# Kernel optimization log

Measured on AMD Instinct MI355X. Metric: run time of the kernel, lower is better.

## Reference

```python
import jax, jax.numpy as jnp
import numpy as np

EMBED_DIM = 4096
POLY_PTS = 32
POLY_DIM = POLY_PTS * 2  # 64
LN_EPS = 1e-5


def setup_inputs() -> dict:
    key = jax.random.key(0)
    ks = jax.random.split(key, 12)
    B, N, Dmax = 8, 1024, POLY_DIM
    s = 0.02
    return {
        "prompts": jax.random.normal(ks[0], (B, N, Dmax), dtype=jnp.float32),
        "prompt_types": jax.random.randint(ks[1], (B, N), 0, 3, dtype=jnp.int64),
        # point encoder: Linear(2, E)
        "point_w": jax.random.normal(ks[2], (EMBED_DIM, 2), dtype=jnp.float32) * s,
        "point_b": jax.random.normal(ks[3], (EMBED_DIM,), dtype=jnp.float32) * s,
        # box encoder: Linear(4, E)
        "box_w": jax.random.normal(ks[4], (EMBED_DIM, 4), dtype=jnp.float32) * s,
        "box_b": jax.random.normal(ks[5], (EMBED_DIM,), dtype=jnp.float32) * s,
        # polygon encoder: Linear(64,E) -> LayerNorm(E) -> ReLU -> Linear(E,E)
        "poly_w1": jax.random.normal(ks[6], (EMBED_DIM, POLY_DIM), dtype=jnp.float32) * s,
        "poly_b1": jax.random.normal(ks[7], (EMBED_DIM,), dtype=jnp.float32) * s,
        "ln_gamma": jnp.ones((EMBED_DIM,), dtype=jnp.float32),
        "ln_beta": jnp.zeros((EMBED_DIM,), dtype=jnp.float32),
        "poly_w2": jax.random.normal(ks[8], (EMBED_DIM, EMBED_DIM), dtype=jnp.float32) * s,
        "poly_b2": jax.random.normal(ks[9], (EMBED_DIM,), dtype=jnp.float32) * s,
        # type embedding table (3, E)
        "type_emb": jax.random.normal(ks[10], (3, EMBED_DIM), dtype=jnp.float32) * s,
    }


def _layernorm(x, gamma, beta):
    mu = jnp.mean(x, axis=-1, keepdims=True)
    var = jnp.mean(jnp.square(x - mu), axis=-1, keepdims=True)
    return (x - mu) * jax.lax.rsqrt(var + LN_EPS) * gamma + beta


def reference(prompts, prompt_types, point_w, point_b, box_w, box_b,
              poly_w1, poly_b1, ln_gamma, ln_beta, poly_w2, poly_b2, type_emb):
    # Per-type expert encodings computed densely, then selected by type mask
    # (same math as torch's masked gather -> linear -> scatter).
    pt = jnp.einsum('bnd,ed->bne', prompts[..., :2], point_w) + point_b + type_emb[0]
    bx = jnp.einsum('bnd,ed->bne', prompts[..., :4], box_w) + box_b + type_emb[1]
    h = jnp.einsum('bnd,ed->bne', prompts[..., :POLY_DIM], poly_w1) + poly_b1
    h = jax.nn.relu(_layernorm(h, ln_gamma, ln_beta))
    pg = jnp.einsum('bnd,ed->bne', h, poly_w2) + poly_b2 + type_emb[2]
    t = prompt_types[..., None]
    zeros = jnp.zeros_like(pt)
    out = jnp.where(t == 0, pt, zeros) + jnp.where(t == 1, bx, zeros) + jnp.where(t == 2, pg, zeros)
    return out
```

## Files before the change

kernel.cpp:

```cpp
#include <hip/hip_runtime.h>

#define EMBED 4096
#define NTOK 8192
#define LN_EPS 1e-5f

typedef float f4_t __attribute__((ext_vector_type(4)));
typedef __bf16 bf16x8 __attribute__((ext_vector_type(8)));
typedef unsigned short us8_t __attribute__((ext_vector_type(8)));

__device__ __forceinline__ unsigned short f2bf(float f) {
    unsigned int u = __float_as_uint(f);
    u += 0x7fffu + ((u >> 16) & 1u);
    return (unsigned short)(u >> 16);
}

typedef const __attribute__((address_space(1))) unsigned int gas_t;
typedef __attribute__((address_space(3))) unsigned int las_t;

__device__ __forceinline__ void gl_lds16(const void* g, void* l) {
    __builtin_amdgcn_global_load_lds((gas_t*)g, (las_t*)l, 16, 0, 0);
}

__global__ void k_compact(const int* __restrict__ types, int* __restrict__ idx,
                          int* __restrict__ counters) {
    __shared__ int cnt;
    if (threadIdx.x == 0) cnt = 0;
    __syncthreads();
    for (int i = threadIdx.x; i < NTOK; i += 1024) {
        if (types[i] == 2) {
            int s = atomicAdd(&cnt, 1);
            idx[s] = i;
        }
    }
    __syncthreads();
    if (threadIdx.x == 0) {
        counters[0] = cnt;
        counters[1] = (cnt + 127) & ~127;
    }
}

__global__ __launch_bounds__(256) void k_prepG(const float* __restrict__ w1,
                                               const float* __restrict__ b1,
                                               float* __restrict__ G,
                                               float* __restrict__ cbar) {
    int i = blockIdx.x;
    int t = threadIdx.x;
    float part[65];
#pragma unroll
    for (int j = 0; j < 65; ++j) part[j] = 0.f;
    for (int e = t; e < EMBED; e += 256) {
        const f4_t* row4 = (const f4_t*)(w1 + (size_t)e * 64);
        float be = b1[e];
        float ai = (i < 64) ? w1[(size_t)e * 64 + i] : ((i == 64) ? be : 1.f);
#pragma unroll
        for (int q = 0; q < 16; ++q) {
            f4_t r = row4[q];
            part[4 * q + 0] += ai * r.x;
            part[4 * q + 1] += ai * r.y;
            part[4 * q + 2] += ai * r.z;
            part[4 * q + 3] += ai * r.w;
        }
        part[64] += ai * be;
    }
#pragma unroll
    for (int j = 0; j < 65; ++j) {
        float v = part[j];
        v += __shfl_down(v, 32);
        v += __shfl_down(v, 16);
        v += __shfl_down(v, 8);
        v += __shfl_down(v, 4);
        v += __shfl_down(v, 2);
        v += __shfl_down(v, 1);
        part[j] = v;
    }
    __shared__ float sw[4][66];
    int wave = t >> 6, lane = t & 63;
    if (lane == 0) {
#pragma unroll
        for (int j = 0; j < 65; ++j) sw[wave][j] = part[j];
    }
    __syncthreads();
    if (t < 65) {
        float s = (sw[0][t] + sw[1][t] + sw[2][t] + sw[3][t]) * (1.f / 4096.f);
        if (i < 65) G[i * 65 + t] = s;
        else        cbar[t] = s;
    }
}

__global__ __launch_bounds__(256) void k_conv(const float* __restrict__ src,
                                              unsigned short* __restrict__ dst) {
    int i = blockIdx.x * 256 + threadIdx.x;
    const f4_t* in4 = (const f4_t*)src;
    f4_t v0 = in4[(size_t)i * 2];
    f4_t v1 = in4[(size_t)i * 2 + 1];
    us8_t o;
    o[0] = f2bf(v0.x); o[1] = f2bf(v0.y); o[2] = f2bf(v0.z); o[3] = f2bf(v0.w);
    o[4] = f2bf(v1.x); o[5] = f2bf(v1.y); o[6] = f2bf(v1.z); o[7] = f2bf(v1.w);
    *(us8_t*)(dst + (size_t)i * 8) = o;
}

__global__ __launch_bounds__(256) void k_enc01(const float* __restrict__ prompts,
                                               const int* __restrict__ types,
                                               const float* __restrict__ pw,
                                               const float* __restrict__ pb,
                                               const float* __restrict__ bw,
                                               const float* __restrict__ bb,
                                               const float* __restrict__ temb,
                                               float* __restrict__ out) {
    int token = blockIdx.x;
    int ty = types[token];
    if (ty >= 2) return;
    const float* x = prompts + (size_t)token * 64;
    float x0 = x[0], x1 = x[1], x2 = x[2], x3 = x[3];
    f4_t* o4 = (f4_t*)(out + (size_t)token * EMBED);
    int t = threadIdx.x;
    if (ty == 0) {
        const f4_t* w4 = (const f4_t*)pw;
        const f4_t* b4 = (const f4_t*)pb;
        const f4_t* te4 = (const f4_t*)temb;
#pragma unroll
        for (int j = 0; j < 4; ++j) {
            int e4 = t + 256 * j;
            f4_t wa = w4[e4 * 2], wb = w4[e4 * 2 + 1];
            f4_t bv = b4[e4], tv = te4[e4];
            f4_t r;
            r.x = x0 * wa.x + x1 * wa.y + bv.x + tv.x;
            r.y = x0 * wa.z + x1 * wa.w + bv.y + tv.y;
            r.z = x0 * wb.x + x1 * wb.y + bv.z + tv.z;
            r.w = x0 * wb.z + x1 * wb.w + bv.w + tv.w;
            o4[e4] = r;
        }
    } else {
        const f4_t* w4 = (const f4_t*)bw;
        const f4_t* b4 = (const f4_t*)bb;
        const f4_t* te4 = (const f4_t*)(temb + EMBED);
#pragma unroll
        for (int j = 0; j < 4; ++j) {
            int e4 = t + 256 * j;
            f4_t w0 = w4[e4 * 4 + 0], w1v = w4[e4 * 4 + 1];
            f4_t w2v = w4[e4 * 4 + 2], w3v = w4[e4 * 4 + 3];
            f4_t bv = b4[e4], tv = te4[e4];
            f4_t r;
            r.x = x0 * w0.x + x1 * w0.y + x2 * w0.z + x3 * w0.w + bv.x + tv.x;
            r.y = x0 * w1v.x + x1 * w1v.y + x2 * w1v.z + x3 * w1v.w + bv.y + tv.y;
            r.z = x0 * w2v.x + x1 * w2v.y + x2 * w2v.z + x3 * w2v.w + bv.z + tv.z;
            r.w = x0 * w3v.x + x1 * w3v.y + x2 * w3v.z + x3 * w3v.w + bv.w + tv.w;
            o4[e4] = r;
        }
    }
}

__global__ __launch_bounds__(256) void k_stats(const float* __restrict__ prompts,
                                               const int* __restrict__ idx,
                                               const int* __restrict__ counters,
                                               const float* __restrict__ cbar,
                                               const float* __restrict__ G,
                                               float* __restrict__ mu,
                                               float* __restrict__ rstd,
                                               unsigned short* __restrict__ xbuf) {
    int count = counters[0], padded = counters[1];
    int base = blockIdx.x * 4;
    if (base >= padded) return;
    __shared__ float sG[65 * 65];
    __shared__ __align__(16) float xs[4][66];
    int t = threadIdx.x;
    for (int v = t; v < 65 * 65; v += 256) sG[v] = G[v];
    int r = t >> 6, lane = t & 63;
    int m = base + r;
    bool vld = (m < count);
    float xv = vld ? prompts[(size_t)idx[m] * 64 + lane] : 0.f;
    xs[r][lane] = xv;
    if (lane == 0) xs[r][64] = vld ? 1.f : 0.f;
    xbuf[(size_t)m * 64 + lane] = vld ? f2bf(xv) : (unsigned short)0;
    __syncthreads();
    float mu_p, m2_p;
    {
        float xi = xs[r][lane];
        mu_p = cbar[lane] * xi;
        const float* Gr = sG + lane * 65;
        float rd = 0.f;
        for (int j = 0; j < 65; ++j) rd += Gr[j] * xs[r][j];
        m2_p = xi * rd;
    }
    if (lane == 0) {
        float xi = xs[r][64];
        mu_p += cbar[64] * xi;
        const float* Gr = sG + 64 * 65;
        float rd = 0.f;
        for (int j = 0; j < 65; ++j) rd += Gr[j] * xs[r][j];
        m2_p += xi * rd;
    }
    for (int off = 32; off > 0; off >>= 1) {
        mu_p += __shfl_down(mu_p, off);
        m2_p += __shfl_down(m2_p, off);
    }
    if (lane == 0) {
        if (vld) {
            mu[m] = mu_p;
            rstd[m] = rsqrtf(fmaxf(m2_p - mu_p * mu_p, 0.f) + LN_EPS);
        } else {
            mu[m] = 0.f;
            rstd[m] = 0.f;
        }
    }
}

__global__ __launch_bounds__(256) void k_lin1m(const unsigned short* __restrict__ xbuf,
                                               const unsigned short* __restrict__ w1b,
                                               const int* __restrict__ counters,
                                               const float* __restrict__ b1,
                                               const float* __restrict__ gamma,
                                               const float* __restrict__ beta,
                                               const float* __restrict__ mu,
                                               const float* __restrict__ rstd,
                                               unsigned short* __restrict__ hbuf) {
    int padded = counters[1];
    int m0 = blockIdx.y * 128;
    if (m0 >= padded) return;
    int n0 = blockIdx.x * 128;

    __shared__ unsigned short At[128 * 32];
    __shared__ unsigned short Bt[128 * 32];

    int t = threadIdx.x;
    int lane = t & 63, wave = t >> 6;
    int wm = (wave >> 1) * 64;
    int wn = (wave & 1) * 64;

    int srow = t >> 2, skg = t & 3;
    const unsigned short* Ag = xbuf + (size_t)(m0 + srow) * 64 + skg * 8;
    const unsigned short* Bg = w1b + (size_t)(n0 + srow) * 64 + skg * 8;
    char* AtC = (char*)At;
    char* BtC = (char*)Bt;
    int ldsw = (t & ~63) * 16;

    f4_t acc[4][4];
#pragma unroll
    for (int i = 0; i < 4; ++i)
#pragma unroll
        for (int j = 0; j < 4; ++j) acc[i][j] = (f4_t)0.f;

    int fr = lane & 15;
    int quad = lane >> 4;

#pragma unroll
    for (int k0 = 0; k0 < 64; k0 += 32) {
        __syncthreads();
        gl_lds16(Ag + k0,            AtC + ldsw);
        gl_lds16(Ag + 64 * 64 + k0,  AtC + 4096 + ldsw);
        gl_lds16(Bg + k0,            BtC + ldsw);
        gl_lds16(Bg + 64 * 64 + k0,  BtC + 4096 + ldsw);
        __syncthreads();

        bf16x8 a[4], b[4];
#pragma unroll
        for (int i = 0; i < 4; ++i) {
            a[i] = *(const bf16x8*)(AtC + (wm + i * 16 + fr) * 64 + quad * 16);
            b[i] = *(const bf16x8*)(BtC + (wn + i * 16 + fr) * 64 + quad * 16);
        }
#pragma unroll
        for (int i = 0; i < 4; ++i)
#pragma unroll
            for (int j = 0; j < 4; ++j)
                acc[i][j] = __builtin_amdgcn_mfma_f32_16x16x32_bf16(a[i], b[j], acc[i][j], 0, 0, 0);
    }

#pragma unroll
    for (int i = 0; i < 4; ++i) {
#pragma unroll
        for (int r = 0; r < 4; ++r) {
            int grow = m0 + wm + i * 16 + quad * 4 + r;
            float muv = mu[grow], rsv = rstd[grow];
            unsigned short* hrow = hbuf + (size_t)grow * EMBED;
#pragma unroll
            for (int j = 0; j < 4; ++j) {
                int gcol = n0 + wn + j * 16 + fr;
                float h = (acc[i][j][r] + b1[gcol] - muv) * rsv * gamma[gcol] + beta[gcol];
                hrow[gcol] = f2bf(fmaxf(h, 0.f));
            }
        }
    }
}

__global__ __launch_bounds__(256) void k_gemm(const unsigned short* __restrict__ hbuf,
                                              const unsigned short* __restrict__ w2b,
                                              const int* __restrict__ idx,
                                              const int* __restrict__ counters,
                                              const float* __restrict__ b2,
                                              const float* __restrict__ te2,
                                              float* __restrict__ out) {
    int count = counters[0], padded = counters[1];
    int m0 = blockIdx.y * 128;
    if (m0 >= padded) return;
    int n0 = blockIdx.x * 128;

    __shared__ unsigned short At[128 * 32];
    __shared__ unsigned short Bt[128 * 32];

    int t = threadIdx.x;
    int lane = t & 63, wave = t >> 6;
    int wm = (wave >> 1) * 64;
    int wn = (wave & 1) * 64;

    int srow = t >> 2, skg = t & 3;
    const unsigned short* Ag = hbuf + (size_t)(m0 + srow) * EMBED + skg * 8;
    const unsigned short* Bg = w2b + (size_t)(n0 + srow) * EMBED + skg * 8;
    char* AtC = (char*)At;
    char* BtC = (char*)Bt;
    int ldsw = (t & ~63) * 16;

    f4_t acc[4][4];
#pragma unroll
    for (int i = 0; i < 4; ++i)
#pragma unroll
        for (int j = 0; j < 4; ++j) acc[i][j] = (f4_t)0.f;

    int fr = lane & 15;
    int quad = lane >> 4;

    for (int k0 = 0; k0 < EMBED; k0 += 32) {
        __syncthreads();
        gl_lds16(Ag + k0,               AtC + ldsw);
        gl_lds16(Ag + 64 * EMBED + k0,  AtC + 4096 + ldsw);
        gl_lds16(Bg + k0,               BtC + ldsw);
        gl_lds16(Bg + 64 * EMBED + k0,  BtC + 4096 + ldsw);
        __syncthreads();

        bf16x8 a[4], b[4];
#pragma unroll
        for (int i = 0; i < 4; ++i) {
            a[i] = *(const bf16x8*)(AtC + (wm + i * 16 + fr) * 64 + quad * 16);
            b[i] = *(const bf16x8*)(BtC + (wn + i * 16 + fr) * 64 + quad * 16);
        }
#pragma unroll
        for (int i = 0; i < 4; ++i)
#pragma unroll
            for (int j = 0; j < 4; ++j)
                acc[i][j] = __builtin_amdgcn_mfma_f32_16x16x32_bf16(a[i], b[j], acc[i][j], 0, 0, 0);
    }

#pragma unroll
    for (int i = 0; i < 4; ++i) {
#pragma unroll
        for (int r = 0; r < 4; ++r) {
            int grow = m0 + wm + i * 16 + quad * 4 + r;
            if (grow < count) {
                float* orow = out + (size_t)idx[grow] * EMBED;
#pragma unroll
                for (int j = 0; j < 4; ++j) {
                    int gcol = n0 + wn + j * 16 + fr;
                    orow[gcol] = acc[i][j][r] + b2[gcol] + te2[gcol];
                }
            }
        }
    }
}

extern "C" void kernel_launch(void* const* d_in, const int* in_sizes, int n_in,
                              void* d_out, int out_size, void* d_ws, size_t ws_size,
                              hipStream_t stream) {
    const float* prompts  = (const float*)d_in[0];
    const int*   types    = (const int*)d_in[1];
    const float* point_w  = (const float*)d_in[2];
    const float* point_b  = (const float*)d_in[3];
    const float* box_w    = (const float*)d_in[4];
    const float* box_b    = (const float*)d_in[5];
    const float* poly_w1  = (const float*)d_in[6];
    const float* poly_b1  = (const float*)d_in[7];
    const float* ln_g     = (const float*)d_in[8];
    const float* ln_b     = (const float*)d_in[9];
    const float* poly_w2  = (const float*)d_in[10];
    const float* poly_b2  = (const float*)d_in[11];
    const float* type_emb = (const float*)d_in[12];
    float* out = (float*)d_out;

    char* ws = (char*)d_ws;
    int*   counters = (int*)ws;
    int*   idx      = (int*)(ws + 256);
    float* cbar     = (float*)(ws + 33280);
    float* G        = (float*)(ws + 33792);
    float* muarr    = (float*)(ws + 51200);
    float* rstdarr  = (float*)(ws + 84224);
    unsigned short* xbuf = (unsigned short*)(ws + 131072);
    unsigned short* w1b  = (unsigned short*)(ws + 131072 + 1048576);
    unsigned short* w2b  = (unsigned short*)(ws + 2097152);
    unsigned short* hbuf = (unsigned short*)(ws + 2097152 + (size_t)EMBED * EMBED * 2);

    k_compact<<<1, 1024, 0, stream>>>(types, idx, counters);
    k_prepG<<<66, 256, 0, stream>>>(poly_w1, poly_b1, G, cbar);
    k_conv<<<EMBED * EMBED / (256 * 8), 256, 0, stream>>>(poly_w2, w2b);
    k_conv<<<EMBED * 64 / (256 * 8), 256, 0, stream>>>(poly_w1, w1b);
    k_enc01<<<NTOK, 256, 0, stream>>>(prompts, types, point_w, point_b,
                                      box_w, box_b, type_emb, out);
    k_stats<<<NTOK / 4, 256, 0, stream>>>(prompts, idx, counters, cbar, G,
                                          muarr, rstdarr, xbuf);
    k_lin1m<<<dim3(EMBED / 128, NTOK / 128), 256, 0, stream>>>(
        xbuf, w1b, counters, poly_b1, ln_g, ln_b, muarr, rstdarr, hbuf);
    k_gemm<<<dim3(EMBED / 128, NTOK / 128), 256, 0, stream>>>(
        hbuf, w2b, idx, counters, poly_b2, type_emb + 2 * EMBED, out);
}
```

Baseline: 387.0 us.

## Merge prep kernels into two multi-role launches and split G reduction across blocks

```diff
diff --git a/kernel.cpp b/kernel.cpp
--- a/kernel.cpp
+++ b/kernel.cpp
@@ -3,6 +3,7 @@
 #define EMBED 4096
 #define NTOK 8192
 #define LN_EPS 1e-5f
+#define PREP_SEG 4
 
 typedef float f4_t __attribute__((ext_vector_type(4)));
 typedef __bf16 bf16x8 __attribute__((ext_vector_type(8)));
@@ -21,34 +22,55 @@
     __builtin_amdgcn_global_load_lds((gas_t*)g, (las_t*)l, 16, 0, 0);
 }
 
-__global__ void k_compact(const int* __restrict__ types, int* __restrict__ idx,
-                          int* __restrict__ counters) {
+
+__device__ void compact_path(const int* __restrict__ types, int* __restrict__ idx,
+                             int* __restrict__ counters) {
     __shared__ int cnt;
-    if (threadIdx.x == 0) cnt = 0;
+    int t = threadIdx.x;
+    if (t == 0) cnt = 0;
     __syncthreads();
-    for (int i = threadIdx.x; i < NTOK; i += 1024) {
-        if (types[i] == 2) {
-            int s = atomicAdd(&cnt, 1);
-            idx[s] = i;
+    int lane = t & 63;
+    for (int i = t; i < NTOK; i += 256) {
+        bool hit = (types[i] == 2);
+        unsigned long long mask = __ballot(hit);
+        int base = 0;
+        if (lane == 0) base = atomicAdd(&cnt, __popcll(mask));
+        base = __shfl(base, 0);
+        if (hit) {
+            int off = __popcll(mask & ((1ull << lane) - 1ull));
+            idx[base + off] = i;
         }
     }
     __syncthreads();
-    if (threadIdx.x == 0) {
+    if (t == 0) {
         counters[0] = cnt;
         counters[1] = (cnt + 127) & ~127;
     }
 }
 
-__global__ __launch_bounds__(256) void k_prepG(const float* __restrict__ w1,
-                                               const float* __restrict__ b1,
-                                               float* __restrict__ G,
-                                               float* __restrict__ cbar) {
-    int i = blockIdx.x;
+__device__ void conv_path(const float* __restrict__ src,
+                          unsigned short* __restrict__ dst, int b) {
+    int i = b * 256 + threadIdx.x;
+    const f4_t* in4 = (const f4_t*)src;
+    f4_t v0 = in4[(size_t)i * 2];
+    f4_t v1 = in4[(size_t)i * 2 + 1];
+    us8_t o;
+    o[0] = f2bf(v0.x); o[1] = f2bf(v0.y); o[2] = f2bf(v0.z); o[3] = f2bf(v0.w);
+    o[4] = f2bf(v1.x); o[5] = f2bf(v1.y); o[6] = f2bf(v1.z); o[7] = f2bf(v1.w);
+    *(us8_t*)(dst + (size_t)i * 8) = o;
+}
+
+__device__ void prepg_path(const float* __restrict__ w1, const float* __restrict__ b1,
+                           float* __restrict__ G, float* __restrict__ cbar, int pid) {
+    int i = pid % 66;
+    int seg = pid / 66;
     int t = threadIdx.x;
     float part[65];
 #pragma unroll
     for (int j = 0; j < 65; ++j) part[j] = 0.f;
-    for (int e = t; e < EMBED; e += 256) {
+    int eBeg = seg * (EMBED / PREP_SEG);
+    int eEnd = eBeg + (EMBED / PREP_SEG);
+    for (int e = eBeg + t; e < eEnd; e += 256) {
         const f4_t* row4 = (const f4_t*)(w1 + (size_t)e * 64);
         float be = b1[e];
         float ai = (i < 64) ? w1[(size_t)e * 64 + i] : ((i == 64) ? be : 1.f);
@@ -82,32 +104,45 @@
     __syncthreads();
     if (t < 65) {
         float s = (sw[0][t] + sw[1][t] + sw[2][t] + sw[3][t]) * (1.f / 4096.f);
-        if (i < 65) G[i * 65 + t] = s;
-        else        cbar[t] = s;
-    }
-}
-
-__global__ __launch_bounds__(256) void k_conv(const float* __restrict__ src,
-                                              unsigned short* __restrict__ dst) {
-    int i = blockIdx.x * 256 + threadIdx.x;
-    const f4_t* in4 = (const f4_t*)src;
-    f4_t v0 = in4[(size_t)i * 2];
-    f4_t v1 = in4[(size_t)i * 2 + 1];
-    us8_t o;
-    o[0] = f2bf(v0.x); o[1] = f2bf(v0.y); o[2] = f2bf(v0.z); o[3] = f2bf(v0.w);
-    o[4] = f2bf(v1.x); o[5] = f2bf(v1.y); o[6] = f2bf(v1.z); o[7] = f2bf(v1.w);
-    *(us8_t*)(dst + (size_t)i * 8) = o;
-}
-
-__global__ __launch_bounds__(256) void k_enc01(const float* __restrict__ prompts,
-                                               const int* __restrict__ types,
-                                               const float* __restrict__ pw,
-                                               const float* __restrict__ pb,
-                                               const float* __restrict__ bw,
-                                               const float* __restrict__ bb,
-                                               const float* __restrict__ temb,
-                                               float* __restrict__ out) {
-    int token = blockIdx.x;
+        if (i < 65) atomicAdd(&G[i * 65 + t], s);
+        else        atomicAdd(&cbar[t], s);
+    }
+}
+
+#define NB_COMPACT 1
+#define NB_CONVW2 (EMBED * EMBED / 2048)
+#define NB_CONVW1 (EMBED * 64 / 2048)
+#define NB_PREPG (66 * PREP_SEG)
+#define NB_MEGA_A (NB_COMPACT + NB_CONVW2 + NB_CONVW1 + NB_PREPG)
+
+__global__ __launch_bounds__(256) void k_megaA(const int* __restrict__ types,
+                                               int* __restrict__ idx,
+                                               int* __restrict__ counters,
+                                               const float* __restrict__ w1,
+                                               const float* __restrict__ b1,
+                                               const float* __restrict__ w2,
+                                               unsigned short* __restrict__ w1b,
+                                               unsigned short* __restrict__ w2b,
+                                               float* __restrict__ G,
+                                               float* __restrict__ cbar) {
+    int b = blockIdx.x;
+    if (b < NB_COMPACT) { compact_path(types, idx, counters); return; }
+    b -= NB_COMPACT;
+    if (b < NB_CONVW2) { conv_path(w2, w2b, b); return; }
+    b -= NB_CONVW2;
+    if (b < NB_CONVW1) { conv_path(w1, w1b, b); return; }
+    b -= NB_CONVW1;
+    prepg_path(w1, b1, G, cbar, b);
+}
+
+
+__device__ void enc01_path(int token,
+                           const float* __restrict__ prompts,
+                           const int* __restrict__ types,
+                           const float* __restrict__ pw, const float* __restrict__ pb,
+                           const float* __restrict__ bw, const float* __restrict__ bb,
+                           const float* __restrict__ temb,
+                           float* __restrict__ out) {
     int ty = types[token];
     if (ty >= 2) return;
     const float* x = prompts + (size_t)token * 64;
@@ -150,7 +185,80 @@
     }
 }
 
-__global__ __launch_bounds__(256) void k_stats(const float* __restrict__ prompts,
+__device__ void stats_path(int p,
+                           const float* __restrict__ prompts,
+                           const int* __restrict__ idx,
+                           const int* __restrict__ counters,
+                           const float* __restrict__ cbar,
+                           const float* __restrict__ G,
+                           float* __restrict__ mu, float* __restrict__ rstd,
+                           unsigned short* __restrict__ xbuf) {
+    int count = counters[0], padded = counters[1];
+    int base = p * 16;
+    if (base >= padded) return;
+    __shared__ float sG[65 * 65];
+    __shared__ __align__(16) float xs[16][66];
+    int t = threadIdx.x;
+    for (int v = t; v < 65 * 65; v += 256) sG[v] = G[v];
+#pragma unroll
+    for (int q = 0; q < 4; ++q) {
+        int slot = t + q * 256;
+        int r = slot >> 6, k = slot & 63;
+        int m = base + r;
+        bool vld = (m < count);
+        float xv = vld ? prompts[(size_t)idx[m] * 64 + k] : 0.f;
+        xs[r][k] = xv;
+        if (k == 0) xs[r][64] = vld ? 1.f : 0.f;
+        xbuf[(size_t)m * 64 + k] = vld ? f2bf(xv) : (unsigned short)0;
+    }
+    __syncthreads();
+    int wv = t >> 6, lane = t & 63;
+#pragma unroll
+    for (int g = 0; g < 4; ++g) {
+        int r = g * 4 + wv;
+        int m = base + r;
+        float xi = xs[r][lane];
+        float mu_p = cbar[lane] * xi;
+        const float* Gr = sG + lane * 65;
+        float rd = 0.f;
+        for (int j = 0; j < 65; ++j) rd += Gr[j] * xs[r][j];
+        float m2_p = xi * rd;
+        if (lane == 0) {
+            float x64 = xs[r][64];
+            mu_p += cbar[64] * x64;
+            const float* G64 = sG + 64 * 65;
+            float rd2 = 0.f;
+            for (int j = 0; j < 65; ++j) rd2 += G64[j] * xs[r][j];
+            m2_p += x64 * rd2;
+        }
+        for (int off = 32; off > 0; off >>= 1) {
+            mu_p += __shfl_down(mu_p, off);
+            m2_p += __shfl_down(m2_p, off);
+        }
+        if (lane == 0) {
+            if (m < count) {
+                mu[m] = mu_p;
+                rstd[m] = rsqrtf(fmaxf(m2_p - mu_p * mu_p, 0.f) + LN_EPS);
+            } else {
+                mu[m] = 0.f;
+                rstd[m] = 0.f;
+            }
+        }
+    }
+}
+
+#define NB_ENC01 NTOK
+#define NB_STATS (NTOK / 16)
+#define NB_MEGA_B (NB_ENC01 + NB_STATS)
+
+__global__ __launch_bounds__(256) void k_megaB(const float* __restrict__ prompts,
+                                               const int* __restrict__ types,
+                                               const float* __restrict__ pw,
+                                               const float* __restrict__ pb,
+                                               const float* __restrict__ bw,
+                                               const float* __restrict__ bb,
+                                               const float* __restrict__ temb,
+                                               float* __restrict__ out,
                                                const int* __restrict__ idx,
                                                const int* __restrict__ counters,
                                                const float* __restrict__ cbar,
@@ -158,51 +266,12 @@
                                                float* __restrict__ mu,
                                                float* __restrict__ rstd,
                                                unsigned short* __restrict__ xbuf) {
-    int count = counters[0], padded = counters[1];
-    int base = blockIdx.x * 4;
-    if (base >= padded) return;
-    __shared__ float sG[65 * 65];
-    __shared__ __align__(16) float xs[4][66];
-    int t = threadIdx.x;
-    for (int v = t; v < 65 * 65; v += 256) sG[v] = G[v];
-    int r = t >> 6, lane = t & 63;
-    int m = base + r;
-    bool vld = (m < count);
-    float xv = vld ? prompts[(size_t)idx[m] * 64 + lane] : 0.f;
-    xs[r][lane] = xv;
-    if (lane == 0) xs[r][64] = vld ? 1.f : 0.f;
-    xbuf[(size_t)m * 64 + lane] = vld ? f2bf(xv) : (unsigned short)0;
-    __syncthreads();
-    float mu_p, m2_p;
-    {
-        float xi = xs[r][lane];
-        mu_p = cbar[lane] * xi;
-        const float* Gr = sG + lane * 65;
-        float rd = 0.f;
-        for (int j = 0; j < 65; ++j) rd += Gr[j] * xs[r][j];
-        m2_p = xi * rd;
-    }
-    if (lane == 0) {
-        float xi = xs[r][64];
-        mu_p += cbar[64] * xi;
-        const float* Gr = sG + 64 * 65;
-        float rd = 0.f;
-        for (int j = 0; j < 65; ++j) rd += Gr[j] * xs[r][j];
-        m2_p += xi * rd;
-    }
-    for (int off = 32; off > 0; off >>= 1) {
-        mu_p += __shfl_down(mu_p, off);
-        m2_p += __shfl_down(m2_p, off);
-    }
-    if (lane == 0) {
-        if (vld) {
-            mu[m] = mu_p;
-            rstd[m] = rsqrtf(fmaxf(m2_p - mu_p * mu_p, 0.f) + LN_EPS);
-        } else {
-            mu[m] = 0.f;
-            rstd[m] = 0.f;
-        }
-    }
+    int b = blockIdx.x;
+    if (b < NB_ENC01) {
+        enc01_path(b, prompts, types, pw, pb, bw, bb, temb, out);
+        return;
+    }
+    stats_path(b - NB_ENC01, prompts, idx, counters, cbar, G, mu, rstd, xbuf);
 }
 
 __global__ __launch_bounds__(256) void k_lin1m(const unsigned short* __restrict__ xbuf,
@@ -290,9 +359,9 @@
                                               const float* __restrict__ te2,
                                               float* __restrict__ out) {
     int count = counters[0], padded = counters[1];
-    int m0 = blockIdx.y * 128;
+    int m0 = blockIdx.x * 128;
     if (m0 >= padded) return;
-    int n0 = blockIdx.x * 128;
+    int n0 = blockIdx.y * 128;
 
     __shared__ unsigned short At[128 * 32];
     __shared__ unsigned short Bt[128 * 32];
@@ -376,26 +445,26 @@
 
     char* ws = (char*)d_ws;
     int*   counters = (int*)ws;
-    int*   idx      = (int*)(ws + 256);
-    float* cbar     = (float*)(ws + 33280);
-    float* G        = (float*)(ws + 33792);
-    float* muarr    = (float*)(ws + 51200);
-    float* rstdarr  = (float*)(ws + 84224);
+    float* G        = (float*)(ws + 256);
+    float* cbar     = (float*)(ws + 256 + 16912);
+    int*   idx      = (int*)(ws + 18432);
+    float* muarr    = (float*)(ws + 65536);
+    float* rstdarr  = (float*)(ws + 98304);
     unsigned short* xbuf = (unsigned short*)(ws + 131072);
     unsigned short* w1b  = (unsigned short*)(ws + 131072 + 1048576);
     unsigned short* w2b  = (unsigned short*)(ws + 2097152);
     unsigned short* hbuf = (unsigned short*)(ws + 2097152 + (size_t)EMBED * EMBED * 2);
 
-    k_compact<<<1, 1024, 0, stream>>>(types, idx, counters);
-    k_prepG<<<66, 256, 0, stream>>>(poly_w1, poly_b1, G, cbar);
-    k_conv<<<EMBED * EMBED / (256 * 8), 256, 0, stream>>>(poly_w2, w2b);
-    k_conv<<<EMBED * 64 / (256 * 8), 256, 0, stream>>>(poly_w1, w1b);
-    k_enc01<<<NTOK, 256, 0, stream>>>(prompts, types, point_w, point_b,
-                                      box_w, box_b, type_emb, out);
-    k_stats<<<NTOK / 4, 256, 0, stream>>>(prompts, idx, counters, cbar, G,
-                                          muarr, rstdarr, xbuf);
+    hipMemsetAsync(ws, 0, 17664, stream);
+
+    k_megaA<<<NB_MEGA_A, 256, 0, stream>>>(types, idx, counters, poly_w1, poly_b1,
+                                           poly_w2, w1b, w2b, G, cbar);
+    k_megaB<<<NB_MEGA_B, 256, 0, stream>>>(prompts, types, point_w, point_b,
+                                           box_w, box_b, type_emb, out,
+                                           idx, counters, cbar, G,
+                                           muarr, rstdarr, xbuf);
     k_lin1m<<<dim3(EMBED / 128, NTOK / 128), 256, 0, stream>>>(
         xbuf, w1b, counters, poly_b1, ln_g, ln_b, muarr, rstdarr, hbuf);
-    k_gemm<<<dim3(EMBED / 128, NTOK / 128), 256, 0, stream>>>(
+    k_gemm<<<dim3(NTOK / 128, EMBED / 128), 256, 0, stream>>>(
         hbuf, w2b, idx, counters, poly_b2, type_emb + 2 * EMBED, out);
 }
```

After: 445.5 us. 1.15x slower.
